# Kernel optimization log

Measured on AMD Instinct MI355X. Metric: run time of the kernel, lower is better.

Reference implementation:

```python
import jax, jax.numpy as jnp
import numpy as np

N = 50000      # nodes
E = 800000     # edges (before self-loops)
F_IN = 128     # num_node_features
HID = 32       # hidden (per-head dim)
H1 = 4         # heads in conv1
G = 64         # graphs in batch


def setup_inputs() -> dict:
    key = jax.random.key(0)
    ks = jax.random.split(key, 12)
    x = jax.random.normal(ks[0], (N, F_IN), jnp.float32)
    edge_index = jax.random.randint(ks[1], (2, E), 0, N)
    batch = jnp.sort(jax.random.randint(ks[2], (N,), 0, G))
    s = lambda k, shape, fan: jax.random.normal(k, shape, jnp.float32) / np.float32(np.sqrt(fan))
    W1 = s(ks[3], (F_IN, H1 * HID), F_IN)
    att_src1 = s(ks[4], (H1, HID), HID)
    att_dst1 = s(ks[5], (H1, HID), HID)
    b1 = jnp.zeros((H1 * HID,), jnp.float32)
    W2 = s(ks[6], (H1 * HID, HID), H1 * HID)
    att_src2 = s(ks[7], (1, HID), HID)
    att_dst2 = s(ks[8], (1, HID), HID)
    b2 = jnp.zeros((HID,), jnp.float32)
    lin1_w = s(ks[9], (HID, HID // 2), HID)
    lin1_b = jnp.zeros((HID // 2,), jnp.float32)
    lin2_w = s(ks[10], (HID // 2, 1), HID // 2)
    lin2_b = jnp.zeros((1,), jnp.float32)
    return dict(x=x, edge_index=edge_index, batch=batch, W1=W1, att_src1=att_src1,
                att_dst1=att_dst1, b1=b1, W2=W2, att_src2=att_src2, att_dst2=att_dst2,
                b2=b2, lin1_w=lin1_w, lin1_b=lin1_b, lin2_w=lin2_w, lin2_b=lin2_b)


def gat_conv(x, src, dst, W, a_src, a_dst, b, heads, dim):
    # PyG GATConv (eval mode): per-edge attention, segment softmax over dst.
    n = x.shape[0]
    h = (x @ W).reshape(n, heads, dim)                         # [N,H,D]
    alpha_src = (h * a_src).sum(-1)                            # [N,H]
    alpha_dst = (h * a_dst).sum(-1)                            # [N,H]
    alpha = jax.nn.leaky_relu(alpha_src[src] + alpha_dst[dst], 0.2)  # [Etot,H]
    amax = jax.ops.segment_max(alpha, dst, num_segments=n)
    e = jnp.exp(alpha - amax[dst])
    denom = jax.ops.segment_sum(e, dst, num_segments=n)
    coef = e / (denom[dst] + 1e-16)
    out = jax.ops.segment_sum(h[src] * coef[:, :, None], dst, num_segments=n)
    return out.reshape(n, heads * dim) + b                     # concat=True


def reference(x, edge_index, batch, W1, att_src1, att_dst1, b1, W2, att_src2,
              att_dst2, b2, lin1_w, lin1_b, lin2_w, lin2_b):
    n = x.shape[0]
    loops = jnp.arange(n, dtype=edge_index.dtype)              # add_self_loops=True
    src = jnp.concatenate([edge_index[0], loops])
    dst = jnp.concatenate([edge_index[1], loops])
    h = jax.nn.elu(gat_conv(x, src, dst, W1, att_src1, att_dst1, b1, H1, HID))
    h = gat_conv(h, src, dst, W2, att_src2, att_dst2, b2, 1, HID)
    counts = jax.ops.segment_sum(jnp.ones((n,), h.dtype), batch, num_segments=G)
    g = jax.ops.segment_sum(h, batch, num_segments=G) / jnp.maximum(counts, 1.0)[:, None]
    g = jax.nn.elu(g @ lin1_w + lin1_b)
    return g @ lin2_w + lin2_b                                  # [G,1]
```

## Files before the change

kernel.cpp:

```cpp
#include <hip/hip_runtime.h>
#include <math.h>

#define N_NODES 50000
#define N_EDGES 800000
#define ETOT (N_EDGES + N_NODES)
#define NG 64
#define NBUCK 196
#define CHUNK 4096
#define NCHUNK ((ETOT + CHUNK - 1)/CHUNK)
#define SCANN (NBUCK*NCHUNK)
#define GSB ((SCANN + 255)/256)
#define GB1 ((N_NODES + 63)/64)

typedef float vf2 __attribute__((ext_vector_type(2)));
typedef short bf16x8 __attribute__((ext_vector_type(8)));
typedef float f32x4 __attribute__((ext_vector_type(4)));

__device__ __forceinline__ float leaky02(float a){ return a > 0.f ? a : 0.2f*a; }
__device__ __forceinline__ float eluf(float v){ return v > 0.f ? v : expm1f(v); }

__device__ __forceinline__ unsigned pack_bf16(float a, float b){
  unsigned ua = __float_as_uint(a); ua += 0x7fffu + ((ua >> 16) & 1u);
  unsigned ub = __float_as_uint(b); ub += 0x7fffu + ((ub >> 16) & 1u);
  return (ua >> 16) | (ub & 0xffff0000u);
}
__device__ __forceinline__ float bf_lo(unsigned v){ return __uint_as_float(v << 16); }
__device__ __forceinline__ float bf_hi(unsigned v){ return __uint_as_float(v & 0xffff0000u); }

__device__ __forceinline__ unsigned pack_fp8x4(float4 a){
  int v = __builtin_amdgcn_cvt_pk_fp8_f32(a.x, a.y, 0, false);
  v = __builtin_amdgcn_cvt_pk_fp8_f32(a.z, a.w, v, true);
  return (unsigned)v;
}

__global__ __launch_bounds__(256) void k_hist(const int* __restrict__ ei,
    unsigned* __restrict__ cnt, const float* __restrict__ W1, const float* __restrict__ W2,
    unsigned* __restrict__ wt1, unsigned* __restrict__ wt2){
  if (blockIdx.x >= NCHUNK){
    int b = blockIdx.x - NCHUNK;
    int t = threadIdx.x;
    if (t < 64){
      if (b < 128){
        float a = W1[(size_t)(2*t)*128 + b];
        float c = W1[(size_t)(2*t+1)*128 + b];
        wt1[b*64 + t] = pack_bf16(a, c);
      } else {
        int cc = b - 128;
        float a = W2[(size_t)(2*t)*32 + cc];
        float c = W2[(size_t)(2*t+1)*32 + cc];
        wt2[cc*64 + t] = pack_bf16(a, c);
      }
    }
    return;
  }
  __shared__ unsigned hist[NBUCK];
  int tid = threadIdx.x;
  for (int t = tid; t < NBUCK; t += 256) hist[t] = 0;
  __syncthreads();
  int base = blockIdx.x * CHUNK;
  #pragma unroll
  for (int i = 0; i < CHUNK/256; ++i){
    int e = base + i*256 + tid;
    if (e < ETOT){
      int d = (e < N_EDGES) ? ei[N_EDGES + e] : (e - N_EDGES);
      atomicAdd(&hist[d >> 8], 1u);
    }
  }
  __syncthreads();
  for (int t = tid; t < NBUCK; t += 256) cnt[t*NCHUNK + blockIdx.x] = hist[t];
}

__global__ __launch_bounds__(256) void g_scanM(const unsigned* __restrict__ in,
    unsigned* __restrict__ out, int n){
  __shared__ unsigned red[4];
  __shared__ unsigned ts[256];
  int t = threadIdx.x, blk = blockIdx.x, i = blk*256 + t;
  unsigned s = 0;
  for (int j = t; j < blk*256; j += 256) s += in[j];
  #pragma unroll
  for (int o = 32; o >= 1; o >>= 1) s += __shfl_xor(s, o);
  if ((t & 63) == 0) red[t >> 6] = s;
  unsigned v = (i < n) ? in[i] : 0u;
  ts[t] = v;
  __syncthreads();
  unsigned base = red[0] + red[1] + red[2] + red[3];
  for (int o = 1; o < 256; o <<= 1){
    unsigned u = (t >= o) ? ts[t-o] : 0u;
    __syncthreads();
    ts[t] += u;
    __syncthreads();
  }
  if (i < n) out[i] = base + ts[t] - v;
}

__global__ __launch_bounds__(256) void k_pg(const int* __restrict__ ei,
    const unsigned* __restrict__ basev, unsigned* __restrict__ staging,
    const float* __restrict__ x, const unsigned* __restrict__ wt1,
    const float* __restrict__ attS, const float* __restrict__ attD,
    unsigned* __restrict__ h1f, float* __restrict__ asrc, float* __restrict__ adst)
{
  __shared__ unsigned cur[NBUCK];
  __shared__ __align__(16) short xs[64*136];
  __shared__ __align__(16) short wb[128*136];
  int tid = threadIdx.x;

  if (blockIdx.x < NCHUNK){
    for (int t = tid; t < NBUCK; t += 256) cur[t] = basev[t*NCHUNK + blockIdx.x];
    __syncthreads();
    int base = blockIdx.x * CHUNK;
    #pragma unroll
    for (int i = 0; i < CHUNK/256; ++i){
      int e = base + i*256 + tid;
      if (e < ETOT){
        int s, d;
        if (e < N_EDGES){ s = ei[e]; d = ei[N_EDGES + e]; } else { s = d = e - N_EDGES; }
        unsigned pos = atomicAdd(&cur[d >> 8], 1u);
        staging[pos] = (unsigned)s | ((unsigned)(d & 255) << 16);
      }
    }
    return;
  }

  float* Cst = (float*)wb;
  int base = (blockIdx.x - NCHUNK) * 64;
  {
    int row = tid >> 2, q = tid & 3;
    const float* src = x + (size_t)(base + row)*128 + q*32;
    bool valid = (base + row) < N_NODES;
    #pragma unroll
    for (int i = 0; i < 8; ++i){
      float4 v = valid ? *(const float4*)(src + 4*i) : make_float4(0,0,0,0);
      *(uint2*)(&xs[row*136 + q*32 + 4*i]) = make_uint2(pack_bf16(v.x, v.y), pack_bf16(v.z, v.w));
    }
  }
  {
    int c = tid >> 1, h = tid & 1;
    #pragma unroll
    for (int i = 0; i < 8; ++i){
      uint4 v = *(const uint4*)(wt1 + c*64 + h*32 + 4*i);
      *(uint4*)(&wb[c*136 + h*64 + 8*i]) = v;
    }
  }
  __syncthreads();
  int lane = tid & 63, wid = tid >> 6;
  int r = lane & 15, g = lane >> 4;
  bf16x8 afr[4];
  #pragma unroll
  for (int kk = 0; kk < 4; ++kk)
    afr[kk] = *(const bf16x8*)(&xs[(wid*16 + r)*136 + kk*32 + g*8]);
  f32x4 acc[8];
  #pragma unroll
  for (int ct = 0; ct < 8; ++ct){ acc[ct][0]=0.f; acc[ct][1]=0.f; acc[ct][2]=0.f; acc[ct][3]=0.f; }
  #pragma unroll
  for (int ct = 0; ct < 8; ++ct){
    #pragma unroll
    for (int kk = 0; kk < 4; ++kk){
      bf16x8 bfr = *(const bf16x8*)(&wb[(ct*16 + r)*136 + kk*32 + g*8]);
      acc[ct] = __builtin_amdgcn_mfma_f32_16x16x32_bf16(afr[kk], bfr, acc[ct], 0, 0, 0);
    }
  }
  __syncthreads();
  #pragma unroll
  for (int ct = 0; ct < 8; ++ct){
    #pragma unroll
    for (int q = 0; q < 4; ++q)
      Cst[(wid*16 + 4*g + q)*132 + ct*16 + r] = acc[ct][q];
  }
  __syncthreads();
  {
    int row = tid >> 2, hd = tid & 3;
    int grow = base + row;
    if (grow < N_NODES){
      const float* cp = &Cst[row*132 + hd*32];
      const float* aS = attS + hd*32;
      const float* aD = attD + hd*32;
      float ps = 0.f, pd = 0.f;
      unsigned u[8];
      #pragma unroll
      for (int i = 0; i < 8; ++i){
        float4 c4 = *(const float4*)(cp + 4*i);
        ps += c4.x*aS[4*i] + c4.y*aS[4*i+1] + c4.z*aS[4*i+2] + c4.w*aS[4*i+3];
        pd += c4.x*aD[4*i] + c4.y*aD[4*i+1] + c4.z*aD[4*i+2] + c4.w*aD[4*i+3];
        u[i] = pack_fp8x4(c4);
      }
      unsigned* dst = h1f + (size_t)grow*32 + hd*8;
      *(uint4*)(dst)     = make_uint4(u[0], u[1], u[2], u[3]);
      *(uint4*)(dst + 4) = make_uint4(u[4], u[5], u[6], u[7]);
      asrc[grow*4 + hd] = ps;
      adst[grow*4 + hd] = pd;
    }
  }
}

__global__ __launch_bounds__(256) void k_csr(const unsigned* __restrict__ basev,
    const unsigned* __restrict__ staging, unsigned* __restrict__ off,
    int* __restrict__ csr_src){
  __shared__ unsigned ts[256], cur[256];
  int tid = threadIdx.x, b = blockIdx.x;
  unsigned start = basev[b*NCHUNK];
  unsigned end = (b == NBUCK-1) ? (unsigned)ETOT : basev[(b+1)*NCHUNK];
  ts[tid] = 0;
  __syncthreads();
  for (unsigned i = start + tid; i < end; i += 256)
    atomicAdd(&ts[staging[i] >> 16], 1u);
  __syncthreads();
  unsigned v = ts[tid];
  for (int o = 1; o < 256; o <<= 1){
    unsigned u = (tid >= o) ? ts[tid-o] : 0u;
    __syncthreads();
    ts[tid] += u;
    __syncthreads();
  }
  unsigned excl = ts[tid] - v;
  int node = (b << 8) + tid;
  if (node < N_NODES) off[node] = start + excl;
  if (b == 0 && tid == 0) off[N_NODES] = (unsigned)ETOT;
  cur[tid] = excl;
  __syncthreads();
  for (unsigned i = start + tid; i < end; i += 256){
    unsigned p = staging[i];
    unsigned pos = atomicAdd(&cur[p >> 16], 1u);
    csr_src[start + pos] = (int)(p & 0xffffu);
  }
}

__global__ __launch_bounds__(256) void k_conv1(const unsigned* __restrict__ off,
    const int* __restrict__ csr_src, const unsigned* __restrict__ h1f,
    const float* __restrict__ asrc, const float* __restrict__ adst,
    const float* __restrict__ b1, unsigned* __restrict__ helu_b)
{
  __shared__ uint2 st[4][4][66];
  int w    = threadIdx.x >> 6;
  int lane = threadIdx.x & 63;
  int n = blockIdx.x*4 + w;
  if (n >= N_NODES) return;
  unsigned s0 = off[n];
  int deg = (int)(off[n+1] - s0);
  float4 ad = *(const float4*)(adst + (size_t)n*4);
  int cl = lane & 31;
  int h  = cl >> 3;
  const char* hbase = (const char*)h1f + 4*cl;
  float4 acc = make_float4(0,0,0,0);
  float den = 0.f;

  if (deg <= 64){
    unsigned boff = 0;
    float e0=0.f, e1=0.f, e2=0.f, e3=0.f;
    if (lane < deg){
      int idx = csr_src[s0 + lane];
      boff = ((unsigned)idx) << 7;
      float4 as = *(const float4*)(asrc + (size_t)idx*4);
      e0 = __expf(leaky02(as.x + ad.x));
      e1 = __expf(leaky02(as.y + ad.y));
      e2 = __expf(leaky02(as.z + ad.z));
      e3 = __expf(leaky02(as.w + ad.w));
    }
    st[w][0][lane] = make_uint2(__float_as_uint(e0), boff);
    st[w][1][lane] = make_uint2(__float_as_uint(e1), boff);
    st[w][2][lane] = make_uint2(__float_as_uint(e2), boff);
    st[w][3][lane] = make_uint2(__float_as_uint(e3), boff);
    __builtin_amdgcn_wave_barrier();
    int half = lane >> 5;
    const uint2* sp = &st[w][h][half];
    #pragma unroll 8
    for (int i = 0; i < deg; i += 2){
      uint2 p = sp[i];
      float es = __uint_as_float(p.x);
      unsigned hb = *(const unsigned*)(hbase + p.y);
      vf2 p0 = __builtin_amdgcn_cvt_pk_f32_fp8((int)hb, false);
      vf2 p1 = __builtin_amdgcn_cvt_pk_f32_fp8((int)hb, true);
      acc.x += es*p0[0]; acc.y += es*p0[1];
      acc.z += es*p1[0]; acc.w += es*p1[1];
      den += es;
    }
    acc.x += __shfl_xor(acc.x, 32); acc.y += __shfl_xor(acc.y, 32);
    acc.z += __shfl_xor(acc.z, 32); acc.w += __shfl_xor(acc.w, 32);
    den   += __shfl_xor(den, 32);
  } else {
    float adh = (h==0) ? ad.x : (h==1) ? ad.y : (h==2) ? ad.z : ad.w;
    for (int i = 0; i < deg; ++i){
      int s = csr_src[s0 + i];
      float ev = __expf(leaky02(asrc[s*4 + h] + adh));
      unsigned hb = *(const unsigned*)(hbase + (((unsigned)s) << 7));
      vf2 p0 = __builtin_amdgcn_cvt_pk_f32_fp8((int)hb, false);
      vf2 p1 = __builtin_amdgcn_cvt_pk_f32_fp8((int)hb, true);
      acc.x += ev*p0[0]; acc.y += ev*p0[1];
      acc.z += ev*p1[0]; acc.w += ev*p1[1];
      den += ev;
    }
  }
  if (lane < 32){
    float inv = 1.f/(den + 1e-16f);
    float4 bv = ((const float4*)b1)[cl];
    float ox = eluf(acc.x*inv + bv.x), oy = eluf(acc.y*inv + bv.y);
    float oz = eluf(acc.z*inv + bv.z), ow = eluf(acc.w*inv + bv.w);
    *(uint2*)(helu_b + (size_t)n*64 + 2*cl) = make_uint2(pack_bf16(ox, oy), pack_bf16(oz, ow));
  }
}

__global__ __launch_bounds__(256) void k_gemm2(const unsigned* __restrict__ helu_b,
    const unsigned* __restrict__ wt2, const float* __restrict__ attS,
    const float* __restrict__ attD, unsigned* __restrict__ h2b,
    float* __restrict__ asrc, float* __restrict__ adst)
{
  __shared__ __align__(16) short xs[64*136];
  __shared__ __align__(16) float cbuf[64*36];
  short* w2 = (short*)cbuf;
  int tid = threadIdx.x;
  int base = blockIdx.x * 64;
  {
    int row = tid >> 2, q = tid & 3;
    bool valid = (base + row) < N_NODES;
    const unsigned* src = helu_b + (size_t)(base + row)*64 + q*16;
    #pragma unroll
    for (int i = 0; i < 4; ++i){
      uint4 v = valid ? *(const uint4*)(src + 4*i) : make_uint4(0,0,0,0);
      *(uint4*)(&xs[row*136 + q*32 + 8*i]) = v;
    }
  }
  {
    int c = tid >> 3, h = tid & 7;
    uint4 v0 = *(const uint4*)(wt2 + c*64 + h*8);
    uint4 v1 = *(const uint4*)(wt2 + c*64 + h*8 + 4);
    *(uint4*)(&w2[c*136 + h*16])     = v0;
    *(uint4*)(&w2[c*136 + h*16 + 8]) = v1;
  }
  __syncthreads();
  int lane = tid & 63, wid = tid >> 6;
  int r = lane & 15, g = lane >> 4;
  bf16x8 afr[4];
  #pragma unroll
  for (int kk = 0; kk < 4; ++kk)
    afr[kk] = *(const bf16x8*)(&xs[(wid*16 + r)*136 + kk*32 + g*8]);
  f32x4 acc[2];
  #pragma unroll
  for (int ct = 0; ct < 2; ++ct){ acc[ct][0]=0.f; acc[ct][1]=0.f; acc[ct][2]=0.f; acc[ct][3]=0.f; }
  #pragma unroll
  for (int ct = 0; ct < 2; ++ct){
    #pragma unroll
    for (int kk = 0; kk < 4; ++kk){
      bf16x8 bfr = *(const bf16x8*)(&w2[(ct*16 + r)*136 + kk*32 + g*8]);
      acc[ct] = __builtin_amdgcn_mfma_f32_16x16x32_bf16(afr[kk], bfr, acc[ct], 0, 0, 0);
    }
  }
  __syncthreads();
  #pragma unroll
  for (int ct = 0; ct < 2; ++ct){
    #pragma unroll
    for (int q = 0; q < 4; ++q)
      cbuf[(wid*16 + 4*g + q)*36 + ct*16 + r] = acc[ct][q];
  }
  __syncthreads();
  {
    int row = tid >> 2, q = tid & 3;
    int grow = base + row;
    if (grow < N_NODES){
      const float* cp = &cbuf[row*36 + q*8];
      float4 c0 = *(const float4*)(cp);
      float4 c1 = *(const float4*)(cp + 4);
      *(uint4*)(h2b + (size_t)grow*16 + q*4) =
        make_uint4(pack_bf16(c0.x,c0.y), pack_bf16(c0.z,c0.w),
                   pack_bf16(c1.x,c1.y), pack_bf16(c1.z,c1.w));
    }
  }
  if (tid < 64){
    int grow = base + tid;
    if (grow < N_NODES){
      const float* cp = &cbuf[tid*36];
      float ps = 0.f, pd = 0.f;
      #pragma unroll
      for (int i = 0; i < 8; ++i){
        float4 c4 = *(const float4*)(cp + 4*i);
        ps += c4.x*attS[4*i] + c4.y*attS[4*i+1] + c4.z*attS[4*i+2] + c4.w*attS[4*i+3];
        pd += c4.x*attD[4*i] + c4.y*attD[4*i+1] + c4.z*attD[4*i+2] + c4.w*attD[4*i+3];
      }
      asrc[grow] = ps; adst[grow] = pd;
    }
  }
}

__global__ __launch_bounds__(256) void k_conv2(const unsigned* __restrict__ off,
    const int* __restrict__ csr_src, const unsigned* __restrict__ h2b,
    const float* __restrict__ asrc, const float* __restrict__ adst,
    const float* __restrict__ b2, float* __restrict__ hout)
{
  __shared__ uint2 st[4][66];
  int w    = threadIdx.x >> 6;
  int lane = threadIdx.x & 63;
  int n = blockIdx.x*4 + w;
  if (n >= N_NODES) return;
  unsigned s0 = off[n];
  int deg = (int)(off[n+1] - s0);
  float ad = adst[n];
  int cl = lane & 7;
  const char* hbase = (const char*)h2b + 8*cl;
  float4 acc = make_float4(0,0,0,0);
  float den = 0.f;

  if (deg <= 64){
    unsigned boff = 0;
    float e = 0.f;
    if (lane < deg){
      int idx = csr_src[s0 + lane];
      boff = ((unsigned)idx) << 6;
      e = __expf(leaky02(asrc[idx] + ad));
    }
    st[w][lane] = make_uint2(__float_as_uint(e), boff);
    __builtin_amdgcn_wave_barrier();
    int g8 = lane >> 3;
    const uint2* sp = &st[w][g8];
    #pragma unroll 4
    for (int i = 0; i < deg; i += 8){
      uint2 p = sp[i];
      float es = __uint_as_float(p.x);
      uint2 hb = *(const uint2*)(hbase + p.y);
      acc.x += es*bf_lo(hb.x); acc.y += es*bf_hi(hb.x);
      acc.z += es*bf_lo(hb.y); acc.w += es*bf_hi(hb.y);
      den += es;
    }
    #pragma unroll
    for (int mm = 8; mm <= 32; mm <<= 1){
      acc.x += __shfl_xor(acc.x, mm); acc.y += __shfl_xor(acc.y, mm);
      acc.z += __shfl_xor(acc.z, mm); acc.w += __shfl_xor(acc.w, mm);
      den   += __shfl_xor(den, mm);
    }
  } else {
    for (int i = 0; i < deg; ++i){
      int s = csr_src[s0 + i];
      float ev = __expf(leaky02(asrc[s] + ad));
      uint2 hb = *(const uint2*)(hbase + (((unsigned)s) << 6));
      acc.x += ev*bf_lo(hb.x); acc.y += ev*bf_hi(hb.x);
      acc.z += ev*bf_lo(hb.y); acc.w += ev*bf_hi(hb.y);
      den += ev;
    }
  }
  if (lane < 8){
    float inv = 1.f/(den + 1e-16f);
    float4 bv = ((const float4*)b2)[cl];
    float4 o;
    o.x = acc.x*inv + bv.x; o.y = acc.y*inv + bv.y;
    o.z = acc.z*inv + bv.z; o.w = acc.w*inv + bv.w;
    *(float4*)(hout + (size_t)n*32 + 4*cl) = o;
  }
}

__global__ __launch_bounds__(256) void k_pool(const int* __restrict__ batch,
    const float* __restrict__ hout, float* __restrict__ gpart, int* __restrict__ gcnt)
{
  int g = blockIdx.x >> 3, sub = blockIdx.x & 7;
  int a = 0, b = N_NODES;
  while (a < b){ int mid = (a+b)>>1; if (batch[mid] < g) a = mid+1; else b = mid; }
  int lo = a;
  b = N_NODES;
  while (a < b){ int mid = (a+b)>>1; if (batch[mid] < g+1) a = mid+1; else b = mid; }
  int hi = a;
  if (sub == 0 && threadIdx.x == 0) gcnt[g] = hi - lo;
  int c = threadIdx.x & 31, rg = threadIdx.x >> 5;
  float s = 0.f;
  for (int r = lo + sub*8 + rg; r < hi; r += 64) s += hout[(size_t)r*32 + c];
  __shared__ float red[8][32];
  red[rg][c] = s;
  __syncthreads();
  if (rg == 0){
    float t = 0.f;
    #pragma unroll
    for (int k = 0; k < 8; ++k) t += red[k][c];
    gpart[(size_t)blockIdx.x*32 + c] = t;
  }
}

__global__ void k_final(const int* __restrict__ gcnt, const float* __restrict__ gpart,
    const float* __restrict__ l1w, const float* __restrict__ l1b,
    const float* __restrict__ l2w, const float* __restrict__ l2b, float* __restrict__ out)
{
  int t = threadIdx.x;
  if (t >= NG) return;
  float cinv = 1.f / fmaxf((float)gcnt[t], 1.0f);
  float4 gs[8];
  #pragma unroll
  for (int q = 0; q < 8; ++q) gs[q] = make_float4(0,0,0,0);
  #pragma unroll
  for (int p = 0; p < 8; ++p){
    const float4* pp = (const float4*)(gpart + (size_t)(t*8 + p)*32);
    #pragma unroll
    for (int q = 0; q < 8; ++q){
      float4 v = pp[q];
      gs[q].x += v.x; gs[q].y += v.y; gs[q].z += v.z; gs[q].w += v.w;
    }
  }
  float g[32];
  #pragma unroll
  for (int q = 0; q < 8; ++q){
    g[4*q]   = gs[q].x * cinv; g[4*q+1] = gs[q].y * cinv;
    g[4*q+2] = gs[q].z * cinv; g[4*q+3] = gs[q].w * cinv;
  }
  float o = l2b[0];
  #pragma unroll
  for (int k = 0; k < 16; ++k){
    float hv = l1b[k];
    #pragma unroll
    for (int j = 0; j < 32; ++j) hv += g[j]*l1w[j*16 + k];
    o += eluf(hv) * l2w[k];
  }
  out[t] = o;
}

extern "C" void kernel_launch(void* const* d_in, const int* in_sizes, int n_in,
                              void* d_out, int out_size, void* d_ws, size_t ws_size,
                              hipStream_t stream) {
  const float* x     = (const float*)d_in[0];
  const int*   ei    = (const int*)  d_in[1];
  const int*   batch = (const int*)  d_in[2];
  const float* W1    = (const float*)d_in[3];
  const float* attS1 = (const float*)d_in[4];
  const float* attD1 = (const float*)d_in[5];
  const float* b1    = (const float*)d_in[6];
  const float* W2    = (const float*)d_in[7];
  const float* attS2 = (const float*)d_in[8];
  const float* attD2 = (const float*)d_in[9];
  const float* b2    = (const float*)d_in[10];
  const float* l1w   = (const float*)d_in[11];
  const float* l1b   = (const float*)d_in[12];
  const float* l2w   = (const float*)d_in[13];
  const float* l2b   = (const float*)d_in[14];
  float* out = (float*)d_out;

  char* w = (char*)d_ws;
  auto alloc = [&](size_t elems) -> void* {
    void* p = (void*)w;
    w += ((elems*4 + 255)/256)*256;
    return p;
  };
  unsigned* csr_off = (unsigned*)alloc(N_NODES + 1);
  unsigned* cnt     = (unsigned*)alloc(SCANN);
  unsigned* basev   = (unsigned*)alloc(SCANN);
  unsigned* staging = (unsigned*)alloc(ETOT);
  int*      csr_src = (int*)     alloc(ETOT);
  unsigned* wt1g  = (unsigned*)alloc(128*64);
  unsigned* wt2g  = (unsigned*)alloc(32*64);
  unsigned* h1f   = (unsigned*)alloc((size_t)N_NODES*32);
  float*    asrc1 = (float*)alloc((size_t)N_NODES*4);
  float*    adst1 = (float*)alloc((size_t)N_NODES*4);
  unsigned* helu_b= (unsigned*)alloc((size_t)N_NODES*64);
  unsigned* h2b   = (unsigned*)alloc((size_t)N_NODES*16);
  float*    asrc2 = (float*)alloc(N_NODES);
  float*    adst2 = (float*)alloc(N_NODES);
  float*    hout  = (float*)alloc((size_t)N_NODES*32);
  float*    gpart = (float*)alloc(NG*8*32);
  int*      gcnt  = (int*)alloc(NG);

  k_hist  <<<NCHUNK + 160, 256, 0, stream>>>(ei, cnt, W1, W2, wt1g, wt2g);
  g_scanM <<<GSB, 256, 0, stream>>>(cnt, basev, SCANN);
  k_pg    <<<NCHUNK + GB1, 256, 0, stream>>>(ei, basev, staging,
                                             x, wt1g, attS1, attD1, h1f, asrc1, adst1);
  k_csr   <<<NBUCK, 256, 0, stream>>>(basev, staging, csr_off, csr_src);

  k_conv1<<<(N_NODES + 3)/4, 256, 0, stream>>>(csr_off, csr_src, h1f, asrc1, adst1, b1, helu_b);
  k_gemm2<<<(N_NODES + 63)/64, 256, 0, stream>>>(helu_b, wt2g, attS2, attD2, h2b, asrc2, adst2);
  k_conv2<<<(N_NODES + 3)/4, 256, 0, stream>>>(csr_off, csr_src, h2b, asrc2, adst2, b2, hout);
  k_pool <<<NG*8, 256, 0, stream>>>(batch, hout, gpart, gcnt);
  k_final<<<1, 64, 0, stream>>>(gcnt, gpart, l1w, l1b, l2w, l2b, out);
}
```

Measured before the change: 154.4 us.

## Replace global scan with fixed-capacity bucket slots and fuse CSR build into gemm1 kernel

```diff
diff --git a/kernel.cpp b/kernel.cpp
--- a/kernel.cpp
+++ b/kernel.cpp
@@ -8,8 +8,7 @@
 #define NBUCK 196
 #define CHUNK 4096
 #define NCHUNK ((ETOT + CHUNK - 1)/CHUNK)
-#define SCANN (NBUCK*NCHUNK)
-#define GSB ((SCANN + 255)/256)
+#define CAP 5120
 #define GB1 ((N_NODES + 63)/64)
 
 typedef float vf2 __attribute__((ext_vector_type(2)));
@@ -33,8 +32,9 @@
   return (unsigned)v;
 }
 
-__global__ __launch_bounds__(256) void k_hist(const int* __restrict__ ei,
-    unsigned* __restrict__ cnt, const float* __restrict__ W1, const float* __restrict__ W2,
+__global__ __launch_bounds__(256) void k_partA(const int* __restrict__ ei,
+    unsigned* __restrict__ gcur, unsigned* __restrict__ staging,
+    const float* __restrict__ W1, const float* __restrict__ W2,
     unsigned* __restrict__ wt1, unsigned* __restrict__ wt2){
   if (blockIdx.x >= NCHUNK){
     int b = blockIdx.x - NCHUNK;
@@ -53,7 +53,7 @@
     }
     return;
   }
-  __shared__ unsigned hist[NBUCK];
+  __shared__ unsigned hist[NBUCK], cur[NBUCK];
   int tid = threadIdx.x;
   for (int t = tid; t < NBUCK; t += 256) hist[t] = 0;
   __syncthreads();
@@ -67,62 +67,64 @@
     }
   }
   __syncthreads();
-  for (int t = tid; t < NBUCK; t += 256) cnt[t*NCHUNK + blockIdx.x] = hist[t];
-}
-
-__global__ __launch_bounds__(256) void g_scanM(const unsigned* __restrict__ in,
-    unsigned* __restrict__ out, int n){
-  __shared__ unsigned red[4];
-  __shared__ unsigned ts[256];
-  int t = threadIdx.x, blk = blockIdx.x, i = blk*256 + t;
-  unsigned s = 0;
-  for (int j = t; j < blk*256; j += 256) s += in[j];
-  #pragma unroll
-  for (int o = 32; o >= 1; o >>= 1) s += __shfl_xor(s, o);
-  if ((t & 63) == 0) red[t >> 6] = s;
-  unsigned v = (i < n) ? in[i] : 0u;
-  ts[t] = v;
-  __syncthreads();
-  unsigned base = red[0] + red[1] + red[2] + red[3];
-  for (int o = 1; o < 256; o <<= 1){
-    unsigned u = (t >= o) ? ts[t-o] : 0u;
-    __syncthreads();
-    ts[t] += u;
-    __syncthreads();
-  }
-  if (i < n) out[i] = base + ts[t] - v;
-}
-
-__global__ __launch_bounds__(256) void k_pg(const int* __restrict__ ei,
-    const unsigned* __restrict__ basev, unsigned* __restrict__ staging,
+  for (int t = tid; t < NBUCK; t += 256)
+    cur[t] = atomicAdd(&gcur[t], hist[t]);
+  __syncthreads();
+  #pragma unroll
+  for (int i = 0; i < CHUNK/256; ++i){
+    int e = base + i*256 + tid;
+    if (e < ETOT){
+      int s, d;
+      if (e < N_EDGES){ s = ei[e]; d = ei[N_EDGES + e]; } else { s = d = e - N_EDGES; }
+      int bk = d >> 8;
+      unsigned pos = atomicAdd(&cur[bk], 1u);
+      staging[(size_t)bk*CAP + pos] = (unsigned)s | ((unsigned)(d & 255) << 16);
+    }
+  }
+}
+
+__global__ __launch_bounds__(256) void k_cg(const unsigned* __restrict__ gcur,
+    const unsigned* __restrict__ staging, uint2* __restrict__ nfo, int* __restrict__ csr_src,
     const float* __restrict__ x, const unsigned* __restrict__ wt1,
     const float* __restrict__ attS, const float* __restrict__ attD,
     unsigned* __restrict__ h1f, float* __restrict__ asrc, float* __restrict__ adst)
 {
-  __shared__ unsigned cur[NBUCK];
+  __shared__ unsigned ts[256], cur2[256];
   __shared__ __align__(16) short xs[64*136];
   __shared__ __align__(16) short wb[128*136];
   int tid = threadIdx.x;
 
-  if (blockIdx.x < NCHUNK){
-    for (int t = tid; t < NBUCK; t += 256) cur[t] = basev[t*NCHUNK + blockIdx.x];
+  if (blockIdx.x < NBUCK){
+    int b = blockIdx.x;
+    unsigned count = gcur[b];
+    unsigned sbase = (unsigned)b*CAP;
+    ts[tid] = 0;
     __syncthreads();
-    int base = blockIdx.x * CHUNK;
-    #pragma unroll
-    for (int i = 0; i < CHUNK/256; ++i){
-      int e = base + i*256 + tid;
-      if (e < ETOT){
-        int s, d;
-        if (e < N_EDGES){ s = ei[e]; d = ei[N_EDGES + e]; } else { s = d = e - N_EDGES; }
-        unsigned pos = atomicAdd(&cur[d >> 8], 1u);
-        staging[pos] = (unsigned)s | ((unsigned)(d & 255) << 16);
-      }
+    for (unsigned i = tid; i < count; i += 256)
+      atomicAdd(&ts[staging[sbase + i] >> 16], 1u);
+    __syncthreads();
+    unsigned v = ts[tid];
+    for (int o = 1; o < 256; o <<= 1){
+      unsigned u = (tid >= o) ? ts[tid-o] : 0u;
+      __syncthreads();
+      ts[tid] += u;
+      __syncthreads();
+    }
+    unsigned excl = ts[tid] - v;
+    int node = (b << 8) + tid;
+    if (node < N_NODES) nfo[node] = make_uint2(sbase + excl, v);
+    cur2[tid] = excl;
+    __syncthreads();
+    for (unsigned i = tid; i < count; i += 256){
+      unsigned p = staging[sbase + i];
+      unsigned pos = atomicAdd(&cur2[p >> 16], 1u);
+      csr_src[sbase + pos] = (int)(p & 0xffffu);
     }
     return;
   }
 
   float* Cst = (float*)wb;
-  int base = (blockIdx.x - NCHUNK) * 64;
+  int base = (blockIdx.x - NBUCK) * 64;
   {
     int row = tid >> 2, q = tid & 3;
     const float* src = x + (size_t)(base + row)*128 + q*32;
@@ -192,39 +194,7 @@
   }
 }
 
-__global__ __launch_bounds__(256) void k_csr(const unsigned* __restrict__ basev,
-    const unsigned* __restrict__ staging, unsigned* __restrict__ off,
-    int* __restrict__ csr_src){
-  __shared__ unsigned ts[256], cur[256];
-  int tid = threadIdx.x, b = blockIdx.x;
-  unsigned start = basev[b*NCHUNK];
-  unsigned end = (b == NBUCK-1) ? (unsigned)ETOT : basev[(b+1)*NCHUNK];
-  ts[tid] = 0;
-  __syncthreads();
-  for (unsigned i = start + tid; i < end; i += 256)
-    atomicAdd(&ts[staging[i] >> 16], 1u);
-  __syncthreads();
-  unsigned v = ts[tid];
-  for (int o = 1; o < 256; o <<= 1){
-    unsigned u = (tid >= o) ? ts[tid-o] : 0u;
-    __syncthreads();
-    ts[tid] += u;
-    __syncthreads();
-  }
-  unsigned excl = ts[tid] - v;
-  int node = (b << 8) + tid;
-  if (node < N_NODES) off[node] = start + excl;
-  if (b == 0 && tid == 0) off[N_NODES] = (unsigned)ETOT;
-  cur[tid] = excl;
-  __syncthreads();
-  for (unsigned i = start + tid; i < end; i += 256){
-    unsigned p = staging[i];
-    unsigned pos = atomicAdd(&cur[p >> 16], 1u);
-    csr_src[start + pos] = (int)(p & 0xffffu);
-  }
-}
-
-__global__ __launch_bounds__(256) void k_conv1(const unsigned* __restrict__ off,
+__global__ __launch_bounds__(256) void k_conv1(const uint2* __restrict__ nfo,
     const int* __restrict__ csr_src, const unsigned* __restrict__ h1f,
     const float* __restrict__ asrc, const float* __restrict__ adst,
     const float* __restrict__ b1, unsigned* __restrict__ helu_b)
@@ -234,8 +204,9 @@
   int lane = threadIdx.x & 63;
   int n = blockIdx.x*4 + w;
   if (n >= N_NODES) return;
-  unsigned s0 = off[n];
-  int deg = (int)(off[n+1] - s0);
+  uint2 nf = nfo[n];
+  unsigned s0 = nf.x;
+  int deg = (int)nf.y;
   float4 ad = *(const float4*)(adst + (size_t)n*4);
   int cl = lane & 31;
   int h  = cl >> 3;
@@ -379,7 +350,7 @@
   }
 }
 
-__global__ __launch_bounds__(256) void k_conv2(const unsigned* __restrict__ off,
+__global__ __launch_bounds__(256) void k_conv2(const uint2* __restrict__ nfo,
     const int* __restrict__ csr_src, const unsigned* __restrict__ h2b,
     const float* __restrict__ asrc, const float* __restrict__ adst,
     const float* __restrict__ b2, float* __restrict__ hout)
@@ -389,8 +360,9 @@
   int lane = threadIdx.x & 63;
   int n = blockIdx.x*4 + w;
   if (n >= N_NODES) return;
-  unsigned s0 = off[n];
-  int deg = (int)(off[n+1] - s0);
+  uint2 nf = nfo[n];
+  unsigned s0 = nf.x;
+  int deg = (int)nf.y;
   float ad = adst[n];
   int cl = lane & 7;
   const char* hbase = (const char*)h2b + 8*cl;
@@ -531,11 +503,10 @@
     w += ((elems*4 + 255)/256)*256;
     return p;
   };
-  unsigned* csr_off = (unsigned*)alloc(N_NODES + 1);
-  unsigned* cnt     = (unsigned*)alloc(SCANN);
-  unsigned* basev   = (unsigned*)alloc(SCANN);
-  unsigned* staging = (unsigned*)alloc(ETOT);
-  int*      csr_src = (int*)     alloc(ETOT);
+  unsigned* gcur    = (unsigned*)alloc(NBUCK);
+  unsigned* staging = (unsigned*)alloc((size_t)NBUCK*CAP);
+  int*      csr_src = (int*)     alloc((size_t)NBUCK*CAP);
+  uint2*    nfo     = (uint2*)   alloc((size_t)N_NODES*2);
   unsigned* wt1g  = (unsigned*)alloc(128*64);
   unsigned* wt2g  = (unsigned*)alloc(32*64);
   unsigned* h1f   = (unsigned*)alloc((size_t)N_NODES*32);
@@ -549,15 +520,14 @@
   float*    gpart = (float*)alloc(NG*8*32);
   int*      gcnt  = (int*)alloc(NG);
 
-  k_hist  <<<NCHUNK + 160, 256, 0, stream>>>(ei, cnt, W1, W2, wt1g, wt2g);
-  g_scanM <<<GSB, 256, 0, stream>>>(cnt, basev, SCANN);
-  k_pg    <<<NCHUNK + GB1, 256, 0, stream>>>(ei, basev, staging,
-                                             x, wt1g, attS1, attD1, h1f, asrc1, adst1);
-  k_csr   <<<NBUCK, 256, 0, stream>>>(basev, staging, csr_off, csr_src);
-
-  k_conv1<<<(N_NODES + 3)/4, 256, 0, stream>>>(csr_off, csr_src, h1f, asrc1, adst1, b1, helu_b);
+  hipMemsetAsync(gcur, 0, NBUCK*4, stream);
+
+  k_partA<<<NCHUNK + 160, 256, 0, stream>>>(ei, gcur, staging, W1, W2, wt1g, wt2g);
+  k_cg   <<<NBUCK + GB1, 256, 0, stream>>>(gcur, staging, nfo, csr_src,
+                                           x, wt1g, attS1, attD1, h1f, asrc1, adst1);
+  k_conv1<<<(N_NODES + 3)/4, 256, 0, stream>>>(nfo, csr_src, h1f, asrc1, adst1, b1, helu_b);
   k_gemm2<<<(N_NODES + 63)/64, 256, 0, stream>>>(helu_b, wt2g, attS2, attD2, h2b, asrc2, adst2);
-  k_conv2<<<(N_NODES + 3)/4, 256, 0, stream>>>(csr_off, csr_src, h2b, asrc2, adst2, b2, hout);
+  k_conv2<<<(N_NODES + 3)/4, 256, 0, stream>>>(nfo, csr_src, h2b, asrc2, adst2, b2, hout);
   k_pool <<<NG*8, 256, 0, stream>>>(batch, hout, gpart, gcnt);
   k_final<<<1, 64, 0, stream>>>(gcnt, gpart, l1w, l1b, l2w, l2b, out);
 }
```

Measured after the change: 130.4 us, median of 2. -15.6%, faster.
